# Optimization experiments

Measured on AMD Instinct MI355X. Metric: run time of the kernel, lower is better.

## Reference

```python
import jax, jax.numpy as jnp
import numpy as np

N = 120000
CIN = 64
C = 128
H = 8
FF = 1.0          # focusing_factor
EPS = 1e-4
BN_EPS = 1e-3
LN_EPS = 1e-3
GX, GY, GZ = 160, 160, 40  # voxel grid for generating realistic sparse coords


def _bn(x, g, b, m, v):
    # inference-mode BatchNorm1d
    return (x - m) * jax.lax.rsqrt(v + BN_EPS) * g + b


def _ln(x, g, b):
    mu = jnp.mean(x, axis=-1, keepdims=True)
    var = jnp.mean(jnp.square(x - mu), axis=-1, keepdims=True)
    return (x - mu) * jax.lax.rsqrt(var + LN_EPS) * g + b


def _l2(x):
    return jnp.sqrt(jnp.sum(jnp.square(x), axis=-1, keepdims=True))


def _forward(features, indices, nbr, W_pre, b_pre, g_pre, be_pre, m_pre, v_pre,
             Wp1, bp1, g_pe, be_pe, m_pe, v_pe, Wp2, bp2,
             W_qkv, b_qkv, scale_p, W_dwc, b_dwc, W_proj, b_proj, g_n1, b_n1):
    sp = _bn(features @ W_pre + b_pre, g_pre, be_pre, m_pre, v_pre)      # [N,C]
    xyz = indices[:, 1:].astype(sp.dtype)                                # [N,3]
    pe = jax.nn.relu(_bn(xyz @ Wp1 + bp1, g_pe, be_pe, m_pe, v_pe)) @ Wp2 + bp2
    qkv = (sp @ W_qkv + b_qkv).reshape(-1, 3, C)
    q, k, v = qkv[:, 0], qkv[:, 1], qkv[:, 2]
    k = k + pe
    # kernel feature map: ReLU + eps
    q = jax.nn.relu(q) + EPS
    k = jax.nn.relu(k) + EPS
    scale = jax.nn.softplus(scale_p)
    q = q / scale
    k = k / scale
    qn, kn = _l2(q), _l2(k)
    # power-law focusing (focusing_factor <= 6 branch)
    q = q ** FF
    k = k ** FF
    # L2 renormalization back to original norms
    q = q / _l2(q) * qn
    k = k / _l2(k) * kn
    d = C // H
    q = q.reshape(-1, H, d).transpose(1, 0, 2)   # [H,N,d]
    k = k.reshape(-1, H, d).transpose(1, 0, 2)
    v = v.reshape(-1, H, d).transpose(1, 0, 2)
    i = j = q.shape[1]
    z = 1.0 / (jnp.einsum('hic,hc->hi', q, k.sum(axis=1)) + EPS)         # [H,N]
    if i * j * (d + d) > d * d * (i + j):
        kv = jnp.einsum('hjc,hjd->hcd', k, v)                            # [H,d,d]
        x = jnp.einsum('hic,hcd->hid', q, kv) * z[..., None]
    else:
        qk = jnp.einsum('hic,hjc->hij', q, k)
        x = jnp.einsum('hij,hjd->hid', qk, v) * z[..., None]
    x = x.transpose(1, 0, 2).reshape(-1, C)                              # [N,C]
    v_full = v.transpose(1, 0, 2).reshape(-1, C)
    # SubMConv3d(C, C, 3) on v via precomputed neighbor table nbr [N,27] (-1 = absent)
    conv = jnp.zeros_like(x)
    nmax = v_full.shape[0] - 1
    for t in range(27):
        idx = nbr[:, t]
        g = jnp.where((idx >= 0)[:, None], v_full[jnp.clip(idx, 0, nmax)], 0.0)
        conv = conv + g @ W_dwc[t]
    conv = conv + b_dwc
    x = x + conv
    x = x @ W_proj + b_proj
    x = _ln(x + sp, g_n1, b_n1)
    return x


def setup_inputs() -> dict:
    rng = np.random.default_rng(0)
    total = GX * GY * GZ
    lin = rng.choice(total, size=N, replace=False)
    x = lin // (GY * GZ)
    rem = lin % (GY * GZ)
    y = rem // GZ
    z = rem % GZ
    dense = -np.ones(total, dtype=np.int32)
    dense[lin] = np.arange(N, dtype=np.int32)
    cols = []
    for dx in (-1, 0, 1):
        for dy in (-1, 0, 1):
            for dz in (-1, 0, 1):
                nx, ny, nz = x + dx, y + dy, z + dz
                valid = (nx >= 0) & (nx < GX) & (ny >= 0) & (ny < GY) & (nz >= 0) & (nz < GZ)
                nlin = np.clip(nx * GY * GZ + ny * GZ + nz, 0, total - 1)
                cols.append(np.where(valid, dense[nlin], -1).astype(np.int32))
    nbr = np.stack(cols, axis=1)
    indices = np.stack([np.zeros(N, dtype=np.int32), x.astype(np.int32),
                        y.astype(np.int32), z.astype(np.int32)], axis=1)
    key = jax.random.key(0)
    ks = jax.random.split(key, 10)
    rn = lambda k, shape, s=0.05: jax.random.normal(k, shape, jnp.float32) * s
    return {
        'features': jax.random.normal(ks[0], (N, CIN), jnp.float32),
        'indices': jnp.asarray(indices),
        'nbr': jnp.asarray(nbr),
        'W_pre': rn(ks[1], (CIN, C)), 'b_pre': jnp.zeros((C,), jnp.float32),
        'g_pre': jnp.ones((C,), jnp.float32), 'be_pre': jnp.zeros((C,), jnp.float32),
        'm_pre': jnp.zeros((C,), jnp.float32), 'v_pre': jnp.ones((C,), jnp.float32),
        'Wp1': rn(ks[2], (3, C)), 'bp1': jnp.zeros((C,), jnp.float32),
        'g_pe': jnp.ones((C,), jnp.float32), 'be_pe': jnp.zeros((C,), jnp.float32),
        'm_pe': jnp.zeros((C,), jnp.float32), 'v_pe': jnp.ones((C,), jnp.float32),
        'Wp2': rn(ks[3], (C, C)), 'bp2': jnp.zeros((C,), jnp.float32),
        'W_qkv': rn(ks[4], (C, 3 * C)), 'b_qkv': jnp.zeros((3 * C,), jnp.float32),
        'scale_p': rn(ks[5], (1, C), 0.5),
        'W_dwc': rn(ks[6], (27, C, C)), 'b_dwc': jnp.zeros((C,), jnp.float32),
        'W_proj': rn(ks[7], (C, C)), 'b_proj': jnp.zeros((C,), jnp.float32),
        'g_n1': jnp.ones((C,), jnp.float32), 'b_n1': jnp.zeros((C,), jnp.float32),
    }


def reference(features, indices, nbr, W_pre, b_pre, g_pre, be_pre, m_pre, v_pre,
              Wp1, bp1, g_pe, be_pe, m_pe, v_pe, Wp2, bp2,
              W_qkv, b_qkv, scale_p, W_dwc, b_dwc, W_proj, b_proj, g_n1, b_n1):
    return _forward(features, indices, nbr, W_pre, b_pre, g_pre, be_pre, m_pre, v_pre,
                    Wp1, bp1, g_pe, be_pe, m_pe, v_pe, Wp2, bp2,
                    W_qkv, b_qkv, scale_p, W_dwc, b_dwc, W_proj, b_proj, g_n1, b_n1)
```

## Files before the change

### kernel.cpp

```cpp
#include <hip/hip_runtime.h>
#include <math.h>

#define EPS 1e-4f
#define BN_EPS 1e-3f
#define LN_EPS 1e-3f

typedef float f32x4 __attribute__((ext_vector_type(4)));
typedef __bf16 bf16x8 __attribute__((ext_vector_type(8)));

__device__ __forceinline__ unsigned int bf16hi_rne(float v){
    unsigned int u = __float_as_uint(v);
    unsigned int r = u + 0x7FFFu + ((u >> 16) & 1u);
    return r & 0xFFFF0000u;
}
__device__ __forceinline__ unsigned int pack_hilo(float v){
    unsigned int hi = bf16hi_rne(v);
    float res = v - __uint_as_float(hi);
    unsigned int u2 = __float_as_uint(res);
    unsigned int r2 = u2 + 0x7FFFu + ((u2 >> 16) & 1u);
    return hi | (r2 >> 16);
}
__device__ __forceinline__ float unpack_hilo(unsigned int p){
    return __uint_as_float(p & 0xFFFF0000u) + __uint_as_float(p << 16);
}
__device__ __forceinline__ f32x4 mfma16(uint4 a, uint4 b, f32x4 c){
    union { uint4 u; bf16x8 v; } A, B;
    A.u = a; B.u = b;
    return __builtin_amdgcn_mfma_f32_16x16x32_bf16(A.v, B.v, c, 0, 0, 0);
}

__global__ __launch_bounds__(256) void k_pre(
    const float* __restrict__ feat, const float* __restrict__ W_pre,
    const float* __restrict__ b_pre, const float* __restrict__ g_pre,
    const float* __restrict__ be_pre, const float* __restrict__ m_pre,
    const float* __restrict__ v_pre, unsigned int* __restrict__ sphl,
    float* __restrict__ accums)
{
    __shared__ __align__(16) float ft[16][64];
    int tid = threadIdx.x;
    int r0 = blockIdx.x * 16;
    if (blockIdx.x == 0){
        for (int i = tid; i < 2176; i += 256) accums[i] = 0.f;
    }
    {
        const float4* src = (const float4*)(feat + (size_t)r0 * 64);
        ((float4*)ft)[tid] = src[tid];
    }
    __syncthreads();
    int c = tid & 127;
    int rg = tid >> 7;
    float acc[8] = {0.f,0.f,0.f,0.f,0.f,0.f,0.f,0.f};
    #pragma unroll
    for (int k = 0; k < 64; k += 4){
        float w0 = W_pre[(k+0)*128 + c];
        float w1 = W_pre[(k+1)*128 + c];
        float w2 = W_pre[(k+2)*128 + c];
        float w3 = W_pre[(k+3)*128 + c];
        #pragma unroll
        for (int j = 0; j < 8; j++){
            float4 a = *(const float4*)&ft[rg*8 + j][k];
            acc[j] += a.x*w0 + a.y*w1 + a.z*w2 + a.w*w3;
        }
    }
    float aa = g_pre[c] * rsqrtf(v_pre[c] + BN_EPS);
    float cc = (b_pre[c] - m_pre[c]) * aa + be_pre[c];
    #pragma unroll
    for (int j = 0; j < 8; j++){
        size_t row = r0 + rg*8 + j;
        sphl[row*128 + c] = pack_hilo(acc[j]*aa + cc);
    }
}

__global__ __launch_bounds__(256) void k_wprep(
    const float* __restrict__ W, unsigned int* __restrict__ whl)
{
    int o = blockIdx.x*256 + threadIdx.x;
    if (o >= 27*128*128) return;
    int k = o & 127; int c = (o >> 7) & 127; int t = o >> 14;
    float v = W[(size_t)((t << 7) + k)*128 + c];
    whl[o] = pack_hilo(v);
}

__global__ __launch_bounds__(256) void k_wprep2(
    const float* __restrict__ Wqkv, const float* __restrict__ Wp2,
    uint4* __restrict__ qwhl)
{
    int o = blockIdx.x*256 + threadIdx.x;
    if (o >= 8192) return;
    int koct = o & 15, col = o >> 4;
    float v[8];
    #pragma unroll
    for (int j = 0; j < 8; j++){
        int k = koct*8 + j;
        v[j] = (col < 384) ? Wqkv[(size_t)k*384 + col] : Wp2[(size_t)k*128 + (col - 384)];
    }
    unsigned int hi[4], lo[4];
    #pragma unroll
    for (int j2 = 0; j2 < 4; j2++){
        float a = v[2*j2], b = v[2*j2+1];
        unsigned int ha = bf16hi_rne(a), hb = bf16hi_rne(b);
        float ra = a - __uint_as_float(ha);
        float rb = b - __uint_as_float(hb);
        hi[j2] = (ha >> 16) | (hb & 0xFFFF0000u);
        lo[j2] = (bf16hi_rne(ra) >> 16) | (bf16hi_rne(rb) & 0xFFFF0000u);
    }
    qwhl[o]        = make_uint4(hi[0],hi[1],hi[2],hi[3]);
    qwhl[8192 + o] = make_uint4(lo[0],lo[1],lo[2],lo[3]);
}

__global__ __launch_bounds__(256) void k_qkv(
    const unsigned int* __restrict__ sphl, const int* __restrict__ indices,
    const float* __restrict__ Wp1, const float* __restrict__ bp1,
    const float* __restrict__ g_pe, const float* __restrict__ be_pe,
    const float* __restrict__ m_pe, const float* __restrict__ v_pe,
    const float* __restrict__ bp2, const uint4* __restrict__ qwhl,
    const float* __restrict__ b_qkv, const float* __restrict__ scale_p,
    float* __restrict__ qb, float* __restrict__ kb, unsigned int* __restrict__ vhl)
{
    __shared__ __align__(16) unsigned int At[2][32*132];
    __shared__ float peout[32*128];
    __shared__ float invs[128];
    __shared__ float xyzs[32][3];
    int tid = threadIdx.x;
    int r0 = blockIdx.x * 32;
    {
        const uint4* src = (const uint4*)(sphl + (size_t)r0*128);
        #pragma unroll
        for (int u = 0; u < 4; u++){
            int i = tid + 256*u;
            int r = i >> 5, cq = i & 31;
            *(uint4*)&At[0][r*132 + cq*4] = src[i];
        }
    }
    if (tid < 96){
        int r = tid / 3, d = tid % 3;
        xyzs[r][d] = (float)indices[(size_t)(r0 + r)*4 + 1 + d];
    }
    if (tid < 128){
        float sx = scale_p[tid];
        float sc = (sx > 20.f) ? sx : log1pf(expf(sx));
        invs[tid] = 1.f / sc;
    }
    __syncthreads();
    #pragma unroll
    for (int u = 0; u < 16; u++){
        int oi = tid + 256*u;
        int r = oi >> 7, c = oi & 127;
        float dot = xyzs[r][0]*Wp1[c] + xyzs[r][1]*Wp1[128+c] + xyzs[r][2]*Wp1[256+c] + bp1[c];
        float aa = g_pe[c] * rsqrtf(v_pe[c] + BN_EPS);
        float t = (dot - m_pe[c])*aa + be_pe[c];
        At[1][r*132 + c] = pack_hilo(fmaxf(t, 0.f));
    }
    __syncthreads();

    int lane = tid & 63;
    int w = tid >> 6;
    int m = lane & 15, kq = lane >> 4;
    const unsigned int* A = &At[w == 3 ? 1 : 0][0];

    uint4 ahi[2][4], alo[2][4];
    #pragma unroll
    for (int rt = 0; rt < 2; rt++){
        #pragma unroll
        for (int ks = 0; ks < 4; ks++){
            const unsigned int* ap = &A[(rt*16 + m)*132 + ks*32 + kq*8];
            uint4 a0 = *(const uint4*)ap;
            uint4 a1 = *(const uint4*)(ap + 4);
            uint4 h, l;
            h.x = __builtin_amdgcn_perm(a0.y, a0.x, 0x07060302u);
            h.y = __builtin_amdgcn_perm(a0.w, a0.z, 0x07060302u);
            h.z = __builtin_amdgcn_perm(a1.y, a1.x, 0x07060302u);
            h.w = __builtin_amdgcn_perm(a1.w, a1.z, 0x07060302u);
            l.x = __builtin_amdgcn_perm(a0.y, a0.x, 0x05040100u);
            l.y = __builtin_amdgcn_perm(a0.w, a0.z, 0x05040100u);
            l.z = __builtin_amdgcn_perm(a1.y, a1.x, 0x05040100u);
            l.w = __builtin_amdgcn_perm(a1.w, a1.z, 0x05040100u);
            ahi[rt][ks] = h; alo[rt][ks] = l;
        }
    }

    f32x4 acc[2][8];
    #pragma unroll
    for (int rt = 0; rt < 2; rt++)
        #pragma unroll
        for (int ct = 0; ct < 8; ct++)
            acc[rt][ct] = (f32x4){0.f,0.f,0.f,0.f};

    int colg = w * 128;
    #pragma unroll
    for (int ct = 0; ct < 8; ct++){
        #pragma unroll
        for (int ks = 0; ks < 4; ks++){
            int bu = (colg + ct*16 + m)*16 + ks*4 + kq;
            uint4 bhi = qwhl[bu];
            uint4 blo = qwhl[8192 + bu];
            #pragma unroll
            for (int rt = 0; rt < 2; rt++){
                acc[rt][ct] = mfma16(ahi[rt][ks], bhi, acc[rt][ct]);
                acc[rt][ct] = mfma16(alo[rt][ks], bhi, acc[rt][ct]);
                acc[rt][ct] = mfma16(ahi[rt][ks], blo, acc[rt][ct]);
            }
        }
    }

    if (w == 3){
        #pragma unroll
        for (int ct = 0; ct < 8; ct++){
            int col = ct*16 + m;
            float bp = bp2[col];
            #pragma unroll
            for (int rt = 0; rt < 2; rt++){
                #pragma unroll
                for (int reg = 0; reg < 4; reg++){
                    int row = rt*16 + kq*4 + reg;
                    peout[row*128 + col] = acc[rt][ct][reg] + bp;
                }
            }
        }
    }
    __syncthreads();
    if (w == 0){
        #pragma unroll
        for (int ct = 0; ct < 8; ct++){
            int col = ct*16 + m;
            float bq = b_qkv[col], inv = invs[col];
            #pragma unroll
            for (int rt = 0; rt < 2; rt++){
                #pragma unroll
                for (int reg = 0; reg < 4; reg++){
                    int row = rt*16 + kq*4 + reg;
                    float v = acc[rt][ct][reg] + bq;
                    qb[(size_t)(r0 + row)*128 + col] = (fmaxf(v, 0.f) + EPS) * inv;
                }
            }
        }
    } else if (w == 1){
        #pragma unroll
        for (int ct = 0; ct < 8; ct++){
            int col = ct*16 + m;
            float bk = b_qkv[128 + col], inv = invs[col];
            #pragma unroll
            for (int rt = 0; rt < 2; rt++){
                #pragma unroll
                for (int reg = 0; reg < 4; reg++){
                    int row = rt*16 + kq*4 + reg;
                    float v = acc[rt][ct][reg] + bk + peout[row*128 + col];
                    kb[(size_t)(r0 + row)*128 + col] = (fmaxf(v, 0.f) + EPS) * inv;
                }
            }
        }
    } else if (w == 2){
        #pragma unroll
        for (int ct = 0; ct < 8; ct++){
            int col = ct*16 + m;
            float bv = b_qkv[256 + col];
            #pragma unroll
            for (int rt = 0; rt < 2; rt++){
                #pragma unroll
                for (int reg = 0; reg < 4; reg++){
                    int row = rt*16 + kq*4 + reg;
                    vhl[(size_t)(r0 + row)*128 + col] = pack_hilo(acc[rt][ct][reg] + bv);
                }
            }
        }
    }
}

__global__ __launch_bounds__(256) void k_red(
    const float* __restrict__ kb, const unsigned int* __restrict__ vhl,
    float* __restrict__ ksum, float* __restrict__ kvm, int ntiles)
{
    __shared__ __align__(16) float kt[16][128];
    __shared__ __align__(16) unsigned int vt[16][128];
    int tid = threadIdx.x;
    int he = tid & 127, fh = tid >> 7;
    int h = he >> 4;
    float akv[8] = {0,0,0,0,0,0,0,0};
    float aks = 0.f;
    for (int ti = blockIdx.x; ti < ntiles; ti += gridDim.x){
        size_t base = (size_t)ti * 16 * 128;
        const float4* ks_ = (const float4*)(kb + base);
        const uint4* vs_ = (const uint4*)(vhl + base);
        float4* kd = (float4*)&kt[0][0];
        uint4* vd = (uint4*)&vt[0][0];
        __syncthreads();
        kd[tid] = ks_[tid]; kd[tid + 256] = ks_[tid + 256];
        vd[tid] = vs_[tid]; vd[tid + 256] = vs_[tid + 256];
        __syncthreads();
        #pragma unroll 4
        for (int r = 0; r < 16; r++){
            float kval = kt[r][he];
            const unsigned int* vr = &vt[r][h*16 + fh*8];
            #pragma unroll
            for (int j = 0; j < 8; j++){
                akv[j] += kval * unpack_hilo(vr[j]);
            }
            if (fh == 0) aks += kval;
        }
    }
    #pragma unroll
    for (int j = 0; j < 8; j++) atomicAdd(&kvm[he*16 + fh*8 + j], akv[j]);
    if (fh == 0) atomicAdd(&ksum[he], aks);
}

__global__ __launch_bounds__(256) void k_conv(
    const unsigned int* __restrict__ vhl, const int* __restrict__ nbr,
    const unsigned int* __restrict__ whl, const float* __restrict__ b_dwc,
    float* __restrict__ xb)
{
    __shared__ __align__(16) unsigned int vt[64*128];
    __shared__ int nbT[27*64];
    int tid = threadIdx.x;
    int r0 = blockIdx.x * 64;
    for (int i = tid; i < 27*64; i += 256){
        int t = i >> 6, r = i & 63;
        nbT[i] = nbr[(size_t)(r0 + r)*27 + t];
    }
    int lane = tid & 63;
    int w    = tid >> 6;
    int m    = lane & 15;
    int h    = lane >> 4;
    int sw   = m & 7;
    int tr   = tid >> 5, tc = tid & 31;
    int colbase = w * 32;

    f32x4 acc[4][2];
    #pragma unroll
    for (int rb = 0; rb < 4; rb++)
        #pragma unroll
        for (int cbi = 0; cbi < 2; cbi++)
            acc[rb][cbi] = (f32x4){0.f,0.f,0.f,0.f};

    const unsigned int* bbase0 = whl + ((size_t)(colbase      + m) << 7);
    const unsigned int* bbase1 = whl + ((size_t)(colbase + 16 + m) << 7);

    for (int t = 0; t < 27; t++){
        __syncthreads();
        #pragma unroll
        for (int s = 0; s < 8; s++){
            int r = tr + 8*s;
            int idx = nbT[t*64 + r];
            uint4 val = make_uint4(0u,0u,0u,0u);
            if (idx >= 0) val = *(const uint4*)&vhl[(size_t)idx*128 + tc*4];
            *(uint4*)&vt[r*128 + (((tc ^ (r & 7)) << 2))] = val;
        }
        __syncthreads();
        const unsigned int* bt0 = bbase0 + ((size_t)t << 14);
        const unsigned int* bt1 = bbase1 + ((size_t)t << 14);
        #pragma unroll
        for (int ks = 0; ks < 4; ks++){
            const unsigned int* bp0 = bt0 + ks*32 + h*8;
            const unsigned int* bp1 = bt1 + ks*32 + h*8;
            uint4 b00 = *(const uint4*)bp0;
            uint4 b01 = *(const uint4*)(bp0 + 4);
            uint4 b10 = *(const uint4*)bp1;
            uint4 b11 = *(const uint4*)(bp1 + 4);
            int G = ks*8 + h*2;
            int offA0 = ((G     ^ sw) << 2);
            int offA1 = (((G+1) ^ sw) << 2);
            uint4 aq[4][2];
            #pragma unroll
            for (int rb = 0; rb < 4; rb++){
                const unsigned int* ap = &vt[(rb*16 + m)*128];
                aq[rb][0] = *(const uint4*)&ap[offA0];
                aq[rb][1] = *(const uint4*)&ap[offA1];
            }
            uint4 ahi[4], alo[4];
            #pragma unroll
            for (int rb = 0; rb < 4; rb++){
                ahi[rb].x = __builtin_amdgcn_perm(aq[rb][0].y, aq[rb][0].x, 0x07060302u);
                ahi[rb].y = __builtin_amdgcn_perm(aq[rb][0].w, aq[rb][0].z, 0x07060302u);
                ahi[rb].z = __builtin_amdgcn_perm(aq[rb][1].y, aq[rb][1].x, 0x07060302u);
                ahi[rb].w = __builtin_amdgcn_perm(aq[rb][1].w, aq[rb][1].z, 0x07060302u);
                alo[rb].x = __builtin_amdgcn_perm(aq[rb][0].y, aq[rb][0].x, 0x05040100u);
                alo[rb].y = __builtin_amdgcn_perm(aq[rb][0].w, aq[rb][0].z, 0x05040100u);
                alo[rb].z = __builtin_amdgcn_perm(aq[rb][1].y, aq[rb][1].x, 0x05040100u);
                alo[rb].w = __builtin_amdgcn_perm(aq[rb][1].w, aq[rb][1].z, 0x05040100u);
            }
            {
                uint4 bhi, blo;
                bhi.x = __builtin_amdgcn_perm(b00.y, b00.x, 0x07060302u);
                bhi.y = __builtin_amdgcn_perm(b00.w, b00.z, 0x07060302u);
                bhi.z = __builtin_amdgcn_perm(b01.y, b01.x, 0x07060302u);
                bhi.w = __builtin_amdgcn_perm(b01.w, b01.z, 0x07060302u);
                blo.x = __builtin_amdgcn_perm(b00.y, b00.x, 0x05040100u);
                blo.y = __builtin_amdgcn_perm(b00.w, b00.z, 0x05040100u);
                blo.z = __builtin_amdgcn_perm(b01.y, b01.x, 0x05040100u);
                blo.w = __builtin_amdgcn_perm(b01.w, b01.z, 0x05040100u);
                #pragma unroll
                for (int rb = 0; rb < 4; rb++){
                    acc[rb][0] = mfma16(ahi[rb], bhi, acc[rb][0]);
                    acc[rb][0] = mfma16(alo[rb], bhi, acc[rb][0]);
                    acc[rb][0] = mfma16(ahi[rb], blo, acc[rb][0]);
                }
            }
            {
                uint4 bhi, blo;
                bhi.x = __builtin_amdgcn_perm(b10.y, b10.x, 0x07060302u);
                bhi.y = __builtin_amdgcn_perm(b10.w, b10.z, 0x07060302u);
                bhi.z = __builtin_amdgcn_perm(b11.y, b11.x, 0x07060302u);
                bhi.w = __builtin_amdgcn_perm(b11.w, b11.z, 0x07060302u);
                blo.x = __builtin_amdgcn_perm(b10.y, b10.x, 0x05040100u);
                blo.y = __builtin_amdgcn_perm(b10.w, b10.z, 0x05040100u);
                blo.z = __builtin_amdgcn_perm(b11.y, b11.x, 0x05040100u);
                blo.w = __builtin_amdgcn_perm(b11.w, b11.z, 0x05040100u);
                #pragma unroll
                for (int rb = 0; rb < 4; rb++){
                    acc[rb][1] = mfma16(ahi[rb], bhi, acc[rb][1]);
                    acc[rb][1] = mfma16(alo[rb], bhi, acc[rb][1]);
                    acc[rb][1] = mfma16(ahi[rb], blo, acc[rb][1]);
                }
            }
        }
    }
    #pragma unroll
    for (int cbi = 0; cbi < 2; cbi++){
        int col = colbase + cbi*16 + m;
        float bias = b_dwc[col];
        f32x4* a = (cbi == 0) ? nullptr : nullptr; (void)a;
        #pragma unroll
        for (int rb = 0; rb < 4; rb++){
            #pragma unroll
            for (int rr = 0; rr < 4; rr++){
                size_t row = (size_t)r0 + rb*16 + h*4 + rr;
                xb[row*128 + col] = ((cbi == 0) ? acc[rb][0][rr] : acc[rb][1][rr]) + bias;
            }
        }
    }
}

__global__ __launch_bounds__(256) void k_out(
    const float* __restrict__ xb, const float* __restrict__ qb,
    const float* __restrict__ ksum, const float* __restrict__ kvm,
    const float* __restrict__ W_proj, const float* __restrict__ b_proj,
    const unsigned int* __restrict__ sphl, const float* __restrict__ g_n1,
    const float* __restrict__ b_n1, float* __restrict__ out)
{
    __shared__ __align__(16) float yt[16][128];
    __shared__ __align__(16) float qt[16][128];
    __shared__ float kvl[2048];
    __shared__ float ksl[128];
    int tid = threadIdx.x;
    int r0 = blockIdx.x * 16;
    {
        const float4* srcy = (const float4*)(xb + (size_t)r0 * 128);
        const float4* srcq = (const float4*)(qb + (size_t)r0 * 128);
        float4* dsty = (float4*)&yt[0][0];
        float4* dstq = (float4*)&qt[0][0];
        dsty[tid] = srcy[tid]; dsty[tid + 256] = srcy[tid + 256];
        dstq[tid] = srcq[tid]; dstq[tid + 256] = srcq[tid + 256];
    }
    #pragma unroll
    for (int u = 0; u < 8; u++) kvl[tid + 256*u] = kvm[tid + 256*u];
    if (tid < 128) ksl[tid] = ksum[tid];
    __syncthreads();

    int c2 = (tid & 63) * 2;
    int rg = tid >> 6;
    {
        int h = c2 >> 4, f0 = c2 & 15;
        float kv0[16], kv1[16], ks[16];
        #pragma unroll
        for (int e = 0; e < 16; e++){
            kv0[e] = kvl[(h*16 + e)*16 + f0];
            kv1[e] = kvl[(h*16 + e)*16 + f0 + 1];
            ks[e]  = ksl[h*16 + e];
        }
        float y[4][2];
        #pragma unroll
        for (int j = 0; j < 4; j++){
            int r = rg*4 + j;
            float zd = 0.f, x0 = 0.f, x1 = 0.f;
            #pragma unroll
            for (int e = 0; e < 16; e++){
                float qe = qt[r][h*16 + e];
                zd += qe * ks[e];
                x0 += qe * kv0[e];
                x1 += qe * kv1[e];
            }
            float iz = 1.f / (zd + EPS);
            y[j][0] = x0*iz + yt[r][c2];
            y[j][1] = x1*iz + yt[r][c2+1];
        }
        #pragma unroll
        for (int j = 0; j < 4; j++){
            yt[rg*4 + j][c2]     = y[j][0];
            yt[rg*4 + j][c2 + 1] = y[j][1];
        }
    }
    __syncthreads();
    float acc[4][2] = {{0,0},{0,0},{0,0},{0,0}};
    for (int k = 0; k < 128; k += 4){
        float2 w0 = *(const float2*)&W_proj[(k+0)*128 + c2];
        float2 w1 = *(const float2*)&W_proj[(k+1)*128 + c2];
        float2 w2 = *(const float2*)&W_proj[(k+2)*128 + c2];
        float2 w3 = *(const float2*)&W_proj[(k+3)*128 + c2];
        #pragma unroll
        for (int j = 0; j < 4; j++){
            float4 a = *(const float4*)&yt[rg*4 + j][k];
            acc[j][0] += a.x*w0.x + a.y*w1.x + a.z*w2.x + a.w*w3.x;
            acc[j][1] += a.x*w0.y + a.y*w1.y + a.z*w2.y + a.w*w3.y;
        }
    }
    float bp0 = b_proj[c2], bp1_ = b_proj[c2+1];
    float g0 = g_n1[c2], g1 = g_n1[c2+1], B0 = b_n1[c2], B1 = b_n1[c2+1];
    float z[4][2], s[4], ss[4];
    #pragma unroll
    for (int j = 0; j < 4; j++){
        size_t row = r0 + rg*4 + j;
        uint2 spv = *(const uint2*)&sphl[row*128 + c2];
        float z0 = acc[j][0] + bp0 + unpack_hilo(spv.x);
        float z1 = acc[j][1] + bp1_ + unpack_hilo(spv.y);
        z[j][0] = z0; z[j][1] = z1;
        s[j] = z0 + z1; ss[j] = z0*z0 + z1*z1;
    }
    #pragma unroll
    for (int m = 1; m < 64; m <<= 1){
        #pragma unroll
        for (int j = 0; j < 4; j++){
            s[j]  += __shfl_xor(s[j],  m, 64);
            ss[j] += __shfl_xor(ss[j], m, 64);
        }
    }
    #pragma unroll
    for (int j = 0; j < 4; j++){
        size_t row = r0 + rg*4 + j;
        float mu = s[j] * (1.f/128.f);
        float var = ss[j] * (1.f/128.f) - mu*mu;
        float rstd = rsqrtf(var + LN_EPS);
        float2 o;
        o.x = (z[j][0] - mu)*rstd*g0 + B0;
        o.y = (z[j][1] - mu)*rstd*g1 + B1;
        *(float2*)&out[row*128 + c2] = o;
    }
}

extern "C" void kernel_launch(void* const* d_in, const int* in_sizes, int n_in,
                              void* d_out, int out_size, void* d_ws, size_t ws_size,
                              hipStream_t stream)
{
    const float* feat    = (const float*)d_in[0];
    const int*   indices = (const int*)  d_in[1];
    const int*   nbr     = (const int*)  d_in[2];
    const float* W_pre   = (const float*)d_in[3];
    const float* b_pre   = (const float*)d_in[4];
    const float* g_pre   = (const float*)d_in[5];
    const float* be_pre  = (const float*)d_in[6];
    const float* m_pre   = (const float*)d_in[7];
    const float* v_pre   = (const float*)d_in[8];
    const float* Wp1     = (const float*)d_in[9];
    const float* bp1     = (const float*)d_in[10];
    const float* g_pe    = (const float*)d_in[11];
    const float* be_pe   = (const float*)d_in[12];
    const float* m_pe    = (const float*)d_in[13];
    const float* v_pe    = (const float*)d_in[14];
    const float* Wp2     = (const float*)d_in[15];
    const float* bp2     = (const float*)d_in[16];
    const float* W_qkv   = (const float*)d_in[17];
    const float* b_qkv   = (const float*)d_in[18];
    const float* scale_p = (const float*)d_in[19];
    const float* W_dwc   = (const float*)d_in[20];
    const float* b_dwc   = (const float*)d_in[21];
    const float* W_proj  = (const float*)d_in[22];
    const float* b_proj  = (const float*)d_in[23];
    const float* g_n1    = (const float*)d_in[24];
    const float* b_n1    = (const float*)d_in[25];
    float* out = (float*)d_out;

    int N = in_sizes[0] / 64;
    size_t NC = (size_t)N * 128;
    float* ws   = (float*)d_ws;
    unsigned int* sphl = (unsigned int*)ws;
    float* qb   = ws + NC;
    float* kb   = ws + 2*NC;
    unsigned int* vhl = (unsigned int*)(ws + 3*NC);
    float* ksum = ws + 4*NC;
    float* kvm  = ksum + 128;
    unsigned int* whl = (unsigned int*)(ksum + 2560);
    uint4* qwhl = (uint4*)(whl + 27*128*128);
    float* xb   = kb;

    k_wprep <<<1728, 256, 0, stream>>>(W_dwc, whl);
    k_wprep2<<<32,   256, 0, stream>>>(W_qkv, Wp2, qwhl);
    k_pre   <<<N/16, 256, 0, stream>>>(feat, W_pre, b_pre, g_pre, be_pre, m_pre, v_pre, sphl, ksum);
    k_qkv   <<<N/32, 256, 0, stream>>>(sphl, indices, Wp1, bp1, g_pe, be_pe, m_pe, v_pe,
                                       bp2, qwhl, b_qkv, scale_p, qb, kb, vhl);
    k_red   <<<256,  256, 0, stream>>>(kb, vhl, ksum, kvm, N/16);
    k_conv  <<<N/64, 256, 0, stream>>>(vhl, nbr, whl, b_dwc, xb);
    k_out   <<<N/16, 256, 0, stream>>>(xb, qb, ksum, kvm, W_proj, b_proj, sphl, g_n1, b_n1, out);
}
```

Measured before the change: 1.096 ms.

## Pre-split conv weights and activations into bf16 hi/lo planes, retile conv waves

The conv weight prep now writes separate bf16 hi and lo planes in an MFMA-ready uint4 layout. The conv kernel splits gathered activations into hi/lo shared-memory planes with a rotating bank layout when it stages them, instead of unpacking them with perm instructions per MFMA. The wave tiling changes from 64x32 per wave to 32x64 (2x2 waves), so each A fragment load feeds four column blocks. The per-MFMA permute work is removed, at the cost of more weight-fragment global loads per step. The k_red grid also grows from 256 to 768 blocks.

```diff
diff --git a/kernel.cpp b/kernel.cpp
--- a/kernel.cpp
+++ b/kernel.cpp
@@ -72,13 +72,27 @@
 }
 
 __global__ __launch_bounds__(256) void k_wprep(
-    const float* __restrict__ W, unsigned int* __restrict__ whl)
+    const float* __restrict__ W, uint4* __restrict__ wpl)
 {
     int o = blockIdx.x*256 + threadIdx.x;
-    if (o >= 27*128*128) return;
-    int k = o & 127; int c = (o >> 7) & 127; int t = o >> 14;
-    float v = W[(size_t)((t << 7) + k)*128 + c];
-    whl[o] = pack_hilo(v);
+    if (o >= 27*16*128) return;
+    int col = o & 127; int koct = (o >> 7) & 15; int t = o >> 11;
+    float v[8];
+    #pragma unroll
+    for (int j = 0; j < 8; j++)
+        v[j] = W[((size_t)(t*128 + koct*8 + j))*128 + col];
+    unsigned int hi[4], lo[4];
+    #pragma unroll
+    for (int j2 = 0; j2 < 4; j2++){
+        float a = v[2*j2], b = v[2*j2+1];
+        unsigned int ha = bf16hi_rne(a), hb = bf16hi_rne(b);
+        float ra = a - __uint_as_float(ha);
+        float rb = b - __uint_as_float(hb);
+        hi[j2] = (ha >> 16) | (hb & 0xFFFF0000u);
+        lo[j2] = (bf16hi_rne(ra) >> 16) | (bf16hi_rne(rb) & 0xFFFF0000u);
+    }
+    wpl[((size_t)(t*2+0)*16 + koct)*128 + col] = make_uint4(hi[0],hi[1],hi[2],hi[3]);
+    wpl[((size_t)(t*2+1)*16 + koct)*128 + col] = make_uint4(lo[0],lo[1],lo[2],lo[3]);
 }
 
 __global__ __launch_bounds__(256) void k_wprep2(
@@ -305,10 +319,10 @@
 
 __global__ __launch_bounds__(256) void k_conv(
     const unsigned int* __restrict__ vhl, const int* __restrict__ nbr,
-    const unsigned int* __restrict__ whl, const float* __restrict__ b_dwc,
+    const uint4* __restrict__ wpl, const float* __restrict__ b_dwc,
     float* __restrict__ xb)
 {
-    __shared__ __align__(16) unsigned int vt[64*128];
+    __shared__ unsigned int pl[2][64*64];
     __shared__ int nbT[27*64];
     int tid = threadIdx.x;
     int r0 = blockIdx.x * 64;
@@ -317,22 +331,17 @@
         nbT[i] = nbr[(size_t)(r0 + r)*27 + t];
     }
     int lane = tid & 63;
-    int w    = tid >> 6;
-    int m    = lane & 15;
-    int h    = lane >> 4;
-    int sw   = m & 7;
-    int tr   = tid >> 5, tc = tid & 31;
-    int colbase = w * 32;
-
-    f32x4 acc[4][2];
-    #pragma unroll
-    for (int rb = 0; rb < 4; rb++)
-        #pragma unroll
-        for (int cbi = 0; cbi < 2; cbi++)
+    int w  = tid >> 6;
+    int wr = w >> 1, wc = w & 1;
+    int m  = lane & 15, kq = lane >> 4;
+    int tr = tid >> 5, tc = tid & 31;
+
+    f32x4 acc[2][4];
+    #pragma unroll
+    for (int rb = 0; rb < 2; rb++)
+        #pragma unroll
+        for (int cbi = 0; cbi < 4; cbi++)
             acc[rb][cbi] = (f32x4){0.f,0.f,0.f,0.f};
-
-    const unsigned int* bbase0 = whl + ((size_t)(colbase      + m) << 7);
-    const unsigned int* bbase1 = whl + ((size_t)(colbase + 16 + m) << 7);
 
     for (int t = 0; t < 27; t++){
         __syncthreads();
@@ -340,90 +349,54 @@
         for (int s = 0; s < 8; s++){
             int r = tr + 8*s;
             int idx = nbT[t*64 + r];
-            uint4 val = make_uint4(0u,0u,0u,0u);
-            if (idx >= 0) val = *(const uint4*)&vhl[(size_t)idx*128 + tc*4];
-            *(uint4*)&vt[r*128 + (((tc ^ (r & 7)) << 2))] = val;
+            uint4 p = make_uint4(0u,0u,0u,0u);
+            if (idx >= 0) p = *(const uint4*)&vhl[(size_t)idx*128 + tc*4];
+            unsigned int h0 = __builtin_amdgcn_perm(p.y, p.x, 0x07060302u);
+            unsigned int h1 = __builtin_amdgcn_perm(p.w, p.z, 0x07060302u);
+            unsigned int l0 = __builtin_amdgcn_perm(p.y, p.x, 0x05040100u);
+            unsigned int l1 = __builtin_amdgcn_perm(p.w, p.z, 0x05040100u);
+            int pos = ((tc >> 1) + r) & 15;
+            int u = r*64 + pos*4 + (tc & 1)*2;
+            *(uint2*)&pl[0][u] = make_uint2(h0, h1);
+            *(uint2*)&pl[1][u] = make_uint2(l0, l1);
         }
         __syncthreads();
-        const unsigned int* bt0 = bbase0 + ((size_t)t << 14);
-        const unsigned int* bt1 = bbase1 + ((size_t)t << 14);
+        const uint4* bt = wpl + (size_t)t*2*16*128;
         #pragma unroll
         for (int ks = 0; ks < 4; ks++){
-            const unsigned int* bp0 = bt0 + ks*32 + h*8;
-            const unsigned int* bp1 = bt1 + ks*32 + h*8;
-            uint4 b00 = *(const uint4*)bp0;
-            uint4 b01 = *(const uint4*)(bp0 + 4);
-            uint4 b10 = *(const uint4*)bp1;
-            uint4 b11 = *(const uint4*)(bp1 + 4);
-            int G = ks*8 + h*2;
-            int offA0 = ((G     ^ sw) << 2);
-            int offA1 = (((G+1) ^ sw) << 2);
-            uint4 aq[4][2];
-            #pragma unroll
-            for (int rb = 0; rb < 4; rb++){
-                const unsigned int* ap = &vt[(rb*16 + m)*128];
-                aq[rb][0] = *(const uint4*)&ap[offA0];
-                aq[rb][1] = *(const uint4*)&ap[offA1];
-            }
-            uint4 ahi[4], alo[4];
-            #pragma unroll
-            for (int rb = 0; rb < 4; rb++){
-                ahi[rb].x = __builtin_amdgcn_perm(aq[rb][0].y, aq[rb][0].x, 0x07060302u);
-                ahi[rb].y = __builtin_amdgcn_perm(aq[rb][0].w, aq[rb][0].z, 0x07060302u);
-                ahi[rb].z = __builtin_amdgcn_perm(aq[rb][1].y, aq[rb][1].x, 0x07060302u);
-                ahi[rb].w = __builtin_amdgcn_perm(aq[rb][1].w, aq[rb][1].z, 0x07060302u);
-                alo[rb].x = __builtin_amdgcn_perm(aq[rb][0].y, aq[rb][0].x, 0x05040100u);
-                alo[rb].y = __builtin_amdgcn_perm(aq[rb][0].w, aq[rb][0].z, 0x05040100u);
-                alo[rb].z = __builtin_amdgcn_perm(aq[rb][1].y, aq[rb][1].x, 0x05040100u);
-                alo[rb].w = __builtin_amdgcn_perm(aq[rb][1].w, aq[rb][1].z, 0x05040100u);
-            }
-            {
-                uint4 bhi, blo;
-                bhi.x = __builtin_amdgcn_perm(b00.y, b00.x, 0x07060302u);
-                bhi.y = __builtin_amdgcn_perm(b00.w, b00.z, 0x07060302u);
-                bhi.z = __builtin_amdgcn_perm(b01.y, b01.x, 0x07060302u);
-                bhi.w = __builtin_amdgcn_perm(b01.w, b01.z, 0x07060302u);
-                blo.x = __builtin_amdgcn_perm(b00.y, b00.x, 0x05040100u);
-                blo.y = __builtin_amdgcn_perm(b00.w, b00.z, 0x05040100u);
-                blo.z = __builtin_amdgcn_perm(b01.y, b01.x, 0x05040100u);
-                blo.w = __builtin_amdgcn_perm(b01.w, b01.z, 0x05040100u);
+            int O = ks*4 + kq;
+            uint4 ahi[2], alo[2];
+            #pragma unroll
+            for (int rb = 0; rb < 2; rb++){
+                int ar = wr*32 + rb*16 + m;
+                int pos = (O + ar) & 15;
+                ahi[rb] = *(const uint4*)&pl[0][ar*64 + pos*4];
+                alo[rb] = *(const uint4*)&pl[1][ar*64 + pos*4];
+            }
+            #pragma unroll
+            for (int cbi = 0; cbi < 4; cbi++){
+                int col = wc*64 + cbi*16 + m;
+                uint4 bhi = bt[(size_t)O*128 + col];
+                uint4 blo = bt[(size_t)(16 + O)*128 + col];
                 #pragma unroll
-                for (int rb = 0; rb < 4; rb++){
-                    acc[rb][0] = mfma16(ahi[rb], bhi, acc[rb][0]);
-                    acc[rb][0] = mfma16(alo[rb], bhi, acc[rb][0]);
-                    acc[rb][0] = mfma16(ahi[rb], blo, acc[rb][0]);
+                for (int rb = 0; rb < 2; rb++){
+                    acc[rb][cbi] = mfma16(ahi[rb], bhi, acc[rb][cbi]);
+                    acc[rb][cbi] = mfma16(alo[rb], bhi, acc[rb][cbi]);
+                    acc[rb][cbi] = mfma16(ahi[rb], blo, acc[rb][cbi]);
                 }
             }
-            {
-                uint4 bhi, blo;
-                bhi.x = __builtin_amdgcn_perm(b10.y, b10.x, 0x07060302u);
-                bhi.y = __builtin_amdgcn_perm(b10.w, b10.z, 0x07060302u);
-                bhi.z = __builtin_amdgcn_perm(b11.y, b11.x, 0x07060302u);
-                bhi.w = __builtin_amdgcn_perm(b11.w, b11.z, 0x07060302u);
-                blo.x = __builtin_amdgcn_perm(b10.y, b10.x, 0x05040100u);
-                blo.y = __builtin_amdgcn_perm(b10.w, b10.z, 0x05040100u);
-                blo.z = __builtin_amdgcn_perm(b11.y, b11.x, 0x05040100u);
-                blo.w = __builtin_amdgcn_perm(b11.w, b11.z, 0x05040100u);
-                #pragma unroll
-                for (int rb = 0; rb < 4; rb++){
-                    acc[rb][1] = mfma16(ahi[rb], bhi, acc[rb][1]);
-                    acc[rb][1] = mfma16(alo[rb], bhi, acc[rb][1]);
-                    acc[rb][1] = mfma16(ahi[rb], blo, acc[rb][1]);
-                }
-            }
-        }
-    }
-    #pragma unroll
-    for (int cbi = 0; cbi < 2; cbi++){
-        int col = colbase + cbi*16 + m;
+        }
+    }
+    #pragma unroll
+    for (int cbi = 0; cbi < 4; cbi++){
+        int col = wc*64 + cbi*16 + m;
         float bias = b_dwc[col];
-        f32x4* a = (cbi == 0) ? nullptr : nullptr; (void)a;
-        #pragma unroll
-        for (int rb = 0; rb < 4; rb++){
-            #pragma unroll
-            for (int rr = 0; rr < 4; rr++){
-                size_t row = (size_t)r0 + rb*16 + h*4 + rr;
-                xb[row*128 + col] = ((cbi == 0) ? acc[rb][0][rr] : acc[rb][1][rr]) + bias;
+        #pragma unroll
+        for (int rb = 0; rb < 2; rb++){
+            #pragma unroll
+            for (int reg = 0; reg < 4; reg++){
+                size_t row = (size_t)r0 + wr*32 + rb*16 + kq*4 + reg;
+                xb[row*128 + col] = acc[rb][cbi][reg] + bias;
             }
         }
     }
@@ -576,16 +549,16 @@
     unsigned int* vhl = (unsigned int*)(ws + 3*NC);
     float* ksum = ws + 4*NC;
     float* kvm  = ksum + 128;
-    unsigned int* whl = (unsigned int*)(ksum + 2560);
-    uint4* qwhl = (uint4*)(whl + 27*128*128);
+    uint4* wpl  = (uint4*)(ksum + 2560);
+    uint4* qwhl = (uint4*)(ksum + 2560 + 442368);
     float* xb   = kb;
 
-    k_wprep <<<1728, 256, 0, stream>>>(W_dwc, whl);
+    k_wprep <<<216,  256, 0, stream>>>(W_dwc, wpl);
     k_wprep2<<<32,   256, 0, stream>>>(W_qkv, Wp2, qwhl);
     k_pre   <<<N/16, 256, 0, stream>>>(feat, W_pre, b_pre, g_pre, be_pre, m_pre, v_pre, sphl, ksum);
     k_qkv   <<<N/32, 256, 0, stream>>>(sphl, indices, Wp1, bp1, g_pe, be_pe, m_pe, v_pe,
                                        bp2, qwhl, b_qkv, scale_p, qb, kb, vhl);
-    k_red   <<<256,  256, 0, stream>>>(kb, vhl, ksum, kvm, N/16);
-    k_conv  <<<N/64, 256, 0, stream>>>(vhl, nbr, whl, b_dwc, xb);
+    k_red   <<<768,  256, 0, stream>>>(kb, vhl, ksum, kvm, N/16);
+    k_conv  <<<N/64, 256, 0, stream>>>(vhl, nbr, wpl, b_dwc, xb);
     k_out   <<<N/16, 256, 0, stream>>>(xb, qb, ksum, kvm, W_proj, b_proj, sphl, g_n1, b_n1, out);
 }
```

Result: slower. 1.150 ms (+4.9%).
